# Kernel optimization log

Measured on AMD Instinct MI355X. Metric: run time of the kernel, lower is better.

Reference implementation:

```python
import jax, jax.numpy as jnp
import numpy as np

NUM_SEGMENTS = 4480  # BATCH_SIZE * MAX_ATOMS = 64 * 70
ATOM_DIM = 64
BOND_DIM = 16
N_EDGES = 65536


def setup_inputs() -> dict:
    key = jax.random.key(0)
    k1, k2, k3, k4 = jax.random.split(key, 4)
    atom_feat = jax.random.normal(k1, (NUM_SEGMENTS, ATOM_DIM), dtype=jnp.float32)
    bond_feat = jax.random.normal(k2, (N_EDGES, BOND_DIM), dtype=jnp.float32)
    pair_idx = jax.random.randint(k3, (N_EDGES, 2), 0, NUM_SEGMENTS, dtype=jnp.int64)
    # glorot-uniform style kernel, zero bias (as in add_weight initializers)
    limit = float(np.sqrt(6.0 / (BOND_DIM + ATOM_DIM ** 2)))
    kernel = jax.random.uniform(k4, (BOND_DIM, ATOM_DIM ** 2), dtype=jnp.float32,
                                minval=-limit, maxval=limit)
    bias = jnp.zeros((ATOM_DIM ** 2,), dtype=jnp.float32)
    return {"atom_feat": atom_feat, "bond_feat": bond_feat,
            "pair_idx": pair_idx, "kernel": kernel, "bias": bias}


def reference(atom_feat, bond_feat, pair_idx, kernel, bias):
    atom_dim = atom_feat.shape[-1]
    # dense projection of bond features -> per-edge transform matrices
    bond_transformed = bond_feat @ kernel + bias               # [E, D*D]
    bond_transformed = bond_transformed.reshape(-1, atom_dim, atom_dim)  # [E, D, D]
    # gather neighbor (source) atom features per edge
    neighbor_feat = jnp.take(atom_feat, pair_idx[:, 1].astype(jnp.int32), axis=0)  # [E, D]
    # per-edge matrix-vector product
    messages = jnp.einsum('eij,ej->ei', bond_transformed, neighbor_feat)  # [E, D]
    # scatter-add into destination atoms
    return jax.ops.segment_sum(messages, pair_idx[:, 0].astype(jnp.int32),
                               num_segments=NUM_SEGMENTS)  # [NUM_SEGMENTS, D]
```

## Files before the change

### kernel.cpp

```cpp
#include <hip/hip_runtime.h>

#define NSEG   4480
#define ADIM   64
#define BDIM   16
#define NEDGE  65536
#define GP     1088
#define CAP    128
#define KP     72

#define EB_OFF   (16u << 20)
#define CNT_OFF  (24u << 20)

typedef __bf16 bf16x8 __attribute__((ext_vector_type(8)));
typedef float  f32x4  __attribute__((ext_vector_type(4)));

__device__ __forceinline__ unsigned short f2bf(float f) {
    union { float f; unsigned int i; } c; c.f = f;
    unsigned int x = c.i;
    x += 0x7fffu + ((x >> 16) & 1u);
    return (unsigned short)(x >> 16);
}

__global__ __launch_bounds__(256) void scatter_kernel(
    const int* __restrict__ pair, int* __restrict__ cnt, int2* __restrict__ eb)
{
    const int e  = blockIdx.x * 256 + threadIdx.x;
    const int2 p = ((const int2*)pair)[e];
    const int idx = atomicAdd(&cnt[p.x], 1);
    if (idx < CAP) eb[(size_t)p.x * CAP + idx] = make_int2(e, p.y);
}

__global__ __launch_bounds__(256) void accum_kernel(
    const float* __restrict__ atom,
    const float* __restrict__ bond,
    const int*   __restrict__ cnt,
    const int2*  __restrict__ eb,
    unsigned short* __restrict__ G)
{
    const int t    = threadIdx.x;
    const int lane = t & 63;
    const int d    = blockIdx.x * 4 + (t >> 6);
    const int nc   = cnt[d];
    const int n    = nc < CAP ? nc : CAP;
    const int2* bk = eb + (size_t)d * CAP;

    float g[17];
#pragma unroll
    for (int r = 0; r < 17; ++r) g[r] = 0.f;

    int k = 0;
    for (; k + 2 <= n; k += 2) {
        const int2 es0 = bk[k];
        const int2 es1 = bk[k + 1];
        const float a0 = atom[(size_t)es0.y * ADIM + lane];
        const float a1 = atom[(size_t)es1.y * ADIM + lane];
        const float4* b0p = (const float4*)(bond + (size_t)es0.x * BDIM);
        const float4* b1p = (const float4*)(bond + (size_t)es1.x * BDIM);
        float4 c0 = b0p[0], c1 = b0p[1], c2 = b0p[2], c3 = b0p[3];
        float4 e0 = b1p[0], e1 = b1p[1], e2 = b1p[2], e3 = b1p[3];
        const float bb0[16] = { c0.x,c0.y,c0.z,c0.w, c1.x,c1.y,c1.z,c1.w,
                                c2.x,c2.y,c2.z,c2.w, c3.x,c3.y,c3.z,c3.w };
        const float bb1[16] = { e0.x,e0.y,e0.z,e0.w, e1.x,e1.y,e1.z,e1.w,
                                e2.x,e2.y,e2.z,e2.w, e3.x,e3.y,e3.z,e3.w };
#pragma unroll
        for (int r = 0; r < 16; ++r) g[r] = fmaf(a0, bb0[r], g[r]);
        g[16] += a0;
#pragma unroll
        for (int r = 0; r < 16; ++r) g[r] = fmaf(a1, bb1[r], g[r]);
        g[16] += a1;
    }
    if (k < n) {
        const int2 es = bk[k];
        const float a = atom[(size_t)es.y * ADIM + lane];
        const float4* bp = (const float4*)(bond + (size_t)es.x * BDIM);
        float4 c0 = bp[0], c1 = bp[1], c2 = bp[2], c3 = bp[3];
        const float bb[16] = { c0.x,c0.y,c0.z,c0.w, c1.x,c1.y,c1.z,c1.w,
                               c2.x,c2.y,c2.z,c2.w, c3.x,c3.y,c3.z,c3.w };
#pragma unroll
        for (int r = 0; r < 16; ++r) g[r] = fmaf(a, bb[r], g[r]);
        g[16] += a;
    }

#pragma unroll
    for (int r = 0; r < 17; ++r)
        G[(size_t)d * GP + r * 64 + lane] = f2bf(g[r]);
}

__global__ __launch_bounds__(256) void gemm_kernel(
    const unsigned short* __restrict__ G,
    const float* __restrict__ kern,
    const float* __restrict__ bias,
    float* __restrict__ out)
{
    __shared__ unsigned short Gs[16 * KP];
    __shared__ unsigned short Ws[64 * KP];

    const int t    = threadIdx.x;
    const int lane = t & 63;
    const int w    = t >> 6;
    const int rb   = blockIdx.x * 16;
    const int m    = lane & 15;
    const int quad = lane >> 4;

    const int wi = t >> 2, wq = t & 3;
    const int gr = t >> 3, gq = t & 7;

    f32x4 acc = {0.f, 0.f, 0.f, 0.f};

    float4 wv[4];
    uint4  gv;
    {
        const float4* wp = (const float4*)(kern + (size_t)wi * 64 + wq * 16);
#pragma unroll
        for (int x = 0; x < 4; ++x) wv[x] = wp[x];
        if (t < 128)
            gv = *(const uint4*)(G + (size_t)(rb + gr) * GP + gq * 8);
    }

    for (int r = 0; r < 17; ++r) {
        __syncthreads();
        {
            unsigned short* dst = Ws + wi * KP + wq * 16;
#pragma unroll
            for (int x = 0; x < 4; ++x) {
                float4 v = wv[x];
                dst[x * 4 + 0] = f2bf(v.x);
                dst[x * 4 + 1] = f2bf(v.y);
                dst[x * 4 + 2] = f2bf(v.z);
                dst[x * 4 + 3] = f2bf(v.w);
            }
            if (t < 128) *(uint4*)(Gs + gr * KP + gq * 8) = gv;
        }
        if (r + 1 < 17) {
            const float* wsrc = (r + 1 < 16) ? (kern + (size_t)(r + 1) * 4096)
                                             : bias;
            const float4* wp = (const float4*)(wsrc + (size_t)wi * 64 + wq * 16);
#pragma unroll
            for (int x = 0; x < 4; ++x) wv[x] = wp[x];
            if (t < 128)
                gv = *(const uint4*)(G + (size_t)(rb + gr) * GP
                                       + (r + 1) * 64 + gq * 8);
        }
        __syncthreads();
#pragma unroll
        for (int kk = 0; kk < 2; ++kk) {
            bf16x8 a = *(const bf16x8*)(Gs + m * KP + kk * 32 + quad * 8);
            bf16x8 b = *(const bf16x8*)(Ws + (w * 16 + m) * KP + kk * 32 + quad * 8);
            acc = __builtin_amdgcn_mfma_f32_16x16x32_bf16(a, b, acc, 0, 0, 0);
        }
    }

#pragma unroll
    for (int rr = 0; rr < 4; ++rr)
        out[(size_t)(rb + quad * 4 + rr) * ADIM + w * 16 + m] = acc[rr];
}

extern "C" void kernel_launch(void* const* d_in, const int* in_sizes, int n_in,
                              void* d_out, int out_size, void* d_ws, size_t ws_size,
                              hipStream_t stream) {
    const float* atom = (const float*)d_in[0];
    const float* bond = (const float*)d_in[1];
    const int*   pair = (const int*)  d_in[2];
    const float* kern = (const float*)d_in[3];
    const float* bias = (const float*)d_in[4];

    float* out = (float*)d_out;

    unsigned short* G = (unsigned short*)d_ws;
    int2* eb = (int2*)((char*)d_ws + EB_OFF);
    int*  cnt = (int*)((char*)d_ws + CNT_OFF);

    hipMemsetAsync(cnt, 0, NSEG * sizeof(int), stream);
    scatter_kernel<<<NEDGE / 256, 256, 0, stream>>>(pair, cnt, eb);
    accum_kernel<<<NSEG / 4, 256, 0, stream>>>(atom, bond, cnt, eb, G);
    gemm_kernel<<<NSEG / 16, 256, 0, stream>>>(G, kern, bias, out);
}
```

Measured before the change: 104.4 us.

## Fuse per-destination accumulation and bf16 GEMM into one kernel via shared memory

Merges the accumulation and GEMM kernels into one 1024-thread block handling 16 destinations. Each wave builds its G row in LDS, and four waves then run the MFMA GEMM, reading weights straight from global memory into registers. This removes the global G round trip and one launch. Edge lists are loaded once per wave and broadcast with readlane, and bucket capacity drops from 128 to 64, which risks dropping edges for high-degree nodes. Only 4 of the 16 waves do the GEMM, and each block converts the weights to bf16 again.

```diff
diff --git a/kernel.cpp b/kernel.cpp
--- a/kernel.cpp
+++ b/kernel.cpp
@@ -4,12 +4,13 @@
 #define ADIM   64
 #define BDIM   16
 #define NEDGE  65536
-#define GP     1088
-#define CAP    128
-#define KP     72
+#define DPB    16
+#define NBLK   (NSEG / DPB)
+#define TPB    1024
+#define CAP    64
+#define GSP    1096
 
-#define EB_OFF   (16u << 20)
-#define CNT_OFF  (24u << 20)
+#define CNT_OFF  (4u << 20)
 
 typedef __bf16 bf16x8 __attribute__((ext_vector_type(8)));
 typedef float  f32x4  __attribute__((ext_vector_type(4)));
@@ -21,6 +22,15 @@
     return (unsigned short)(x >> 16);
 }
 
+union U8 { unsigned short u[8]; bf16x8 v; };
+
+__device__ __forceinline__ bf16x8 pack_bf8(float4 a, float4 b) {
+    U8 r;
+    r.u[0] = f2bf(a.x); r.u[1] = f2bf(a.y); r.u[2] = f2bf(a.z); r.u[3] = f2bf(a.w);
+    r.u[4] = f2bf(b.x); r.u[5] = f2bf(b.y); r.u[6] = f2bf(b.z); r.u[7] = f2bf(b.w);
+    return r.v;
+}
+
 __global__ __launch_bounds__(256) void scatter_kernel(
     const int* __restrict__ pair, int* __restrict__ cnt, int2* __restrict__ eb)
 {
@@ -30,129 +40,111 @@
     if (idx < CAP) eb[(size_t)p.x * CAP + idx] = make_int2(e, p.y);
 }
 
-__global__ __launch_bounds__(256) void accum_kernel(
+__global__ __launch_bounds__(TPB) void fused_kernel(
     const float* __restrict__ atom,
     const float* __restrict__ bond,
     const int*   __restrict__ cnt,
     const int2*  __restrict__ eb,
-    unsigned short* __restrict__ G)
-{
-    const int t    = threadIdx.x;
-    const int lane = t & 63;
-    const int d    = blockIdx.x * 4 + (t >> 6);
-    const int nc   = cnt[d];
-    const int n    = nc < CAP ? nc : CAP;
-    const int2* bk = eb + (size_t)d * CAP;
-
-    float g[17];
-#pragma unroll
-    for (int r = 0; r < 17; ++r) g[r] = 0.f;
-
-    int k = 0;
-    for (; k + 2 <= n; k += 2) {
-        const int2 es0 = bk[k];
-        const int2 es1 = bk[k + 1];
-        const float a0 = atom[(size_t)es0.y * ADIM + lane];
-        const float a1 = atom[(size_t)es1.y * ADIM + lane];
-        const float4* b0p = (const float4*)(bond + (size_t)es0.x * BDIM);
-        const float4* b1p = (const float4*)(bond + (size_t)es1.x * BDIM);
-        float4 c0 = b0p[0], c1 = b0p[1], c2 = b0p[2], c3 = b0p[3];
-        float4 e0 = b1p[0], e1 = b1p[1], e2 = b1p[2], e3 = b1p[3];
-        const float bb0[16] = { c0.x,c0.y,c0.z,c0.w, c1.x,c1.y,c1.z,c1.w,
-                                c2.x,c2.y,c2.z,c2.w, c3.x,c3.y,c3.z,c3.w };
-        const float bb1[16] = { e0.x,e0.y,e0.z,e0.w, e1.x,e1.y,e1.z,e1.w,
-                                e2.x,e2.y,e2.z,e2.w, e3.x,e3.y,e3.z,e3.w };
-#pragma unroll
-        for (int r = 0; r < 16; ++r) g[r] = fmaf(a0, bb0[r], g[r]);
-        g[16] += a0;
-#pragma unroll
-        for (int r = 0; r < 16; ++r) g[r] = fmaf(a1, bb1[r], g[r]);
-        g[16] += a1;
-    }
-    if (k < n) {
-        const int2 es = bk[k];
-        const float a = atom[(size_t)es.y * ADIM + lane];
-        const float4* bp = (const float4*)(bond + (size_t)es.x * BDIM);
-        float4 c0 = bp[0], c1 = bp[1], c2 = bp[2], c3 = bp[3];
-        const float bb[16] = { c0.x,c0.y,c0.z,c0.w, c1.x,c1.y,c1.z,c1.w,
-                               c2.x,c2.y,c2.z,c2.w, c3.x,c3.y,c3.z,c3.w };
-#pragma unroll
-        for (int r = 0; r < 16; ++r) g[r] = fmaf(a, bb[r], g[r]);
-        g[16] += a;
-    }
-
-#pragma unroll
-    for (int r = 0; r < 17; ++r)
-        G[(size_t)d * GP + r * 64 + lane] = f2bf(g[r]);
-}
-
-__global__ __launch_bounds__(256) void gemm_kernel(
-    const unsigned short* __restrict__ G,
     const float* __restrict__ kern,
     const float* __restrict__ bias,
-    float* __restrict__ out)
+    float*       __restrict__ out)
 {
-    __shared__ unsigned short Gs[16 * KP];
-    __shared__ unsigned short Ws[64 * KP];
+    __shared__ unsigned short Gs[DPB * GSP];
 
     const int t    = threadIdx.x;
     const int lane = t & 63;
     const int w    = t >> 6;
-    const int rb   = blockIdx.x * 16;
-    const int m    = lane & 15;
-    const int quad = lane >> 4;
+    const int dlo  = blockIdx.x * DPB;
+    const int d    = dlo + w;
 
-    const int wi = t >> 2, wq = t & 3;
-    const int gr = t >> 3, gq = t & 7;
+    {
+        int n = cnt[d];
+        n = n < CAP ? n : CAP;
+        const int2 my = eb[(size_t)d * CAP + lane];
 
-    f32x4 acc = {0.f, 0.f, 0.f, 0.f};
+        float g[17];
+#pragma unroll
+        for (int r = 0; r < 17; ++r) g[r] = 0.f;
 
-    float4 wv[4];
-    uint4  gv;
-    {
-        const float4* wp = (const float4*)(kern + (size_t)wi * 64 + wq * 16);
+        int k = 0;
+        for (; k + 2 <= n; k += 2) {
+            const int e0 = __builtin_amdgcn_readlane(my.x, k);
+            const int s0 = __builtin_amdgcn_readlane(my.y, k);
+            const int e1 = __builtin_amdgcn_readlane(my.x, k + 1);
+            const int s1 = __builtin_amdgcn_readlane(my.y, k + 1);
+            const float a0 = atom[(size_t)s0 * ADIM + lane];
+            const float a1 = atom[(size_t)s1 * ADIM + lane];
+            const float4* b0p = (const float4*)(bond + (size_t)e0 * BDIM);
+            const float4* b1p = (const float4*)(bond + (size_t)e1 * BDIM);
+            const float4 c0 = b0p[0], c1 = b0p[1], c2 = b0p[2], c3 = b0p[3];
+            const float4 d0 = b1p[0], d1 = b1p[1], d2 = b1p[2], d3 = b1p[3];
+            const float bb0[16] = { c0.x,c0.y,c0.z,c0.w, c1.x,c1.y,c1.z,c1.w,
+                                    c2.x,c2.y,c2.z,c2.w, c3.x,c3.y,c3.z,c3.w };
+            const float bb1[16] = { d0.x,d0.y,d0.z,d0.w, d1.x,d1.y,d1.z,d1.w,
+                                    d2.x,d2.y,d2.z,d2.w, d3.x,d3.y,d3.z,d3.w };
 #pragma unroll
-        for (int x = 0; x < 4; ++x) wv[x] = wp[x];
-        if (t < 128)
-            gv = *(const uint4*)(G + (size_t)(rb + gr) * GP + gq * 8);
-    }
-
-    for (int r = 0; r < 17; ++r) {
-        __syncthreads();
-        {
-            unsigned short* dst = Ws + wi * KP + wq * 16;
+            for (int r = 0; r < 16; ++r) g[r] = fmaf(a0, bb0[r], g[r]);
+            g[16] += a0;
 #pragma unroll
-            for (int x = 0; x < 4; ++x) {
-                float4 v = wv[x];
-                dst[x * 4 + 0] = f2bf(v.x);
-                dst[x * 4 + 1] = f2bf(v.y);
-                dst[x * 4 + 2] = f2bf(v.z);
-                dst[x * 4 + 3] = f2bf(v.w);
-            }
-            if (t < 128) *(uint4*)(Gs + gr * KP + gq * 8) = gv;
+            for (int r = 0; r < 16; ++r) g[r] = fmaf(a1, bb1[r], g[r]);
+            g[16] += a1;
         }
-        if (r + 1 < 17) {
-            const float* wsrc = (r + 1 < 16) ? (kern + (size_t)(r + 1) * 4096)
-                                             : bias;
-            const float4* wp = (const float4*)(wsrc + (size_t)wi * 64 + wq * 16);
+        if (k < n) {
+            const int e0 = __builtin_amdgcn_readlane(my.x, k);
+            const int s0 = __builtin_amdgcn_readlane(my.y, k);
+            const float a0 = atom[(size_t)s0 * ADIM + lane];
+            const float4* b0p = (const float4*)(bond + (size_t)e0 * BDIM);
+            const float4 c0 = b0p[0], c1 = b0p[1], c2 = b0p[2], c3 = b0p[3];
+            const float bb0[16] = { c0.x,c0.y,c0.z,c0.w, c1.x,c1.y,c1.z,c1.w,
+                                    c2.x,c2.y,c2.z,c2.w, c3.x,c3.y,c3.z,c3.w };
 #pragma unroll
-            for (int x = 0; x < 4; ++x) wv[x] = wp[x];
-            if (t < 128)
-                gv = *(const uint4*)(G + (size_t)(rb + gr) * GP
-                                       + (r + 1) * 64 + gq * 8);
+            for (int r = 0; r < 16; ++r) g[r] = fmaf(a0, bb0[r], g[r]);
+            g[16] += a0;
         }
-        __syncthreads();
-#pragma unroll
-        for (int kk = 0; kk < 2; ++kk) {
-            bf16x8 a = *(const bf16x8*)(Gs + m * KP + kk * 32 + quad * 8);
-            bf16x8 b = *(const bf16x8*)(Ws + (w * 16 + m) * KP + kk * 32 + quad * 8);
-            acc = __builtin_amdgcn_mfma_f32_16x16x32_bf16(a, b, acc, 0, 0, 0);
-        }
-    }
 
 #pragma unroll
-    for (int rr = 0; rr < 4; ++rr)
-        out[(size_t)(rb + quad * 4 + rr) * ADIM + w * 16 + m] = acc[rr];
+        for (int r = 0; r < 17; ++r)
+            Gs[w * GSP + r * 64 + lane] = f2bf(g[r]);
+    }
+    __syncthreads();
+
+    if (w < 4) {
+        const int m    = lane & 15;
+        const int quad = lane >> 4;
+        const int c    = w * 16 + m;
+        const unsigned short* Ga = Gs + (size_t)m * GSP;
+
+        f32x4 acc = {0.f, 0.f, 0.f, 0.f};
+
+        const float* ks0 = kern + (size_t)c * 64 + quad * 8;
+        float4 x0 = *(const float4*)(ks0);
+        float4 x1 = *(const float4*)(ks0 + 4);
+        float4 y0 = *(const float4*)(ks0 + 32);
+        float4 y1 = *(const float4*)(ks0 + 36);
+
+#pragma unroll
+        for (int r = 0; r < 17; ++r) {
+            float4 nx0, nx1, ny0, ny1;
+            if (r + 1 < 17) {
+                const float* ns = ((r + 1 < 16) ? (kern + (size_t)(r + 1) * 4096)
+                                                : bias)
+                                  + (size_t)c * 64 + quad * 8;
+                nx0 = *(const float4*)(ns);
+                nx1 = *(const float4*)(ns + 4);
+                ny0 = *(const float4*)(ns + 32);
+                ny1 = *(const float4*)(ns + 36);
+            }
+            const bf16x8 a0 = *(const bf16x8*)(Ga + r * 64 + quad * 8);
+            const bf16x8 a1 = *(const bf16x8*)(Ga + r * 64 + 32 + quad * 8);
+            acc = __builtin_amdgcn_mfma_f32_16x16x32_bf16(a0, pack_bf8(x0, x1), acc, 0, 0, 0);
+            acc = __builtin_amdgcn_mfma_f32_16x16x32_bf16(a1, pack_bf8(y0, y1), acc, 0, 0, 0);
+            x0 = nx0; x1 = nx1; y0 = ny0; y1 = ny1;
+        }
+
+#pragma unroll
+        for (int rr = 0; rr < 4; ++rr)
+            out[(size_t)(dlo + quad * 4 + rr) * ADIM + c] = acc[rr];
+    }
 }
 
 extern "C" void kernel_launch(void* const* d_in, const int* in_sizes, int n_in,
@@ -163,15 +155,12 @@
     const int*   pair = (const int*)  d_in[2];
     const float* kern = (const float*)d_in[3];
     const float* bias = (const float*)d_in[4];
-
     float* out = (float*)d_out;
 
-    unsigned short* G = (unsigned short*)d_ws;
-    int2* eb = (int2*)((char*)d_ws + EB_OFF);
+    int2* eb = (int2*)d_ws;
     int*  cnt = (int*)((char*)d_ws + CNT_OFF);
 
     hipMemsetAsync(cnt, 0, NSEG * sizeof(int), stream);
     scatter_kernel<<<NEDGE / 256, 256, 0, stream>>>(pair, cnt, eb);
-    accum_kernel<<<NSEG / 4, 256, 0, stream>>>(atom, bond, cnt, eb, G);
-    gemm_kernel<<<NSEG / 16, 256, 0, stream>>>(G, kern, bias, out);
+    fused_kernel<<<NBLK, TPB, 0, stream>>>(atom, bond, cnt, eb, kern, bias, out);
 }
```

New measurement: 92.19 us. 1.13x faster.
